# Performance work log

Hardware: AMD Instinct MI355X
Metric: run time of the kernel (lower is better)

Reference implementation:

```python
import jax, jax.numpy as jnp
import numpy as np

B, N, IN_DIM = 2, 2048, 512
D_MODEL, N_HEADS, N_CLASSES = 1024, 16, 1024


def sin_pos_encoding(n, d):
    # Matches SinPositionalEncoding buffer pe[:n]
    pos = jnp.arange(n, dtype=jnp.float32)[:, None]
    div = jnp.exp(jnp.arange(0, d, 2, dtype=jnp.float32) * (-np.log(10000.0) / d))
    pe = jnp.zeros((n, d), dtype=jnp.float32)
    pe = pe.at[:, 0::2].set(jnp.sin(pos * div))
    pe = pe.at[:, 1::2].set(jnp.cos(pos * div))
    return pe


def setup_inputs() -> dict:
    key = jax.random.key(0)
    ks = jax.random.split(key, 9)
    s_emb = (2.0 / (IN_DIM + D_MODEL)) ** 0.5
    s_qk = (2.0 / (2 * D_MODEL)) ** 0.5
    s_v = (2.0 / (D_MODEL + 1)) ** 0.5
    s_o = (2.0 / (N_HEADS + D_MODEL)) ** 0.5
    s_dec = (2.0 / (D_MODEL + N_CLASSES)) ** 0.5
    return {
        'X': jax.random.normal(ks[0], (B, N, IN_DIM), dtype=jnp.float32),
        'emb_w': jax.random.normal(ks[1], (IN_DIM, D_MODEL), dtype=jnp.float32) * s_emb,
        'emb_b': jax.random.normal(ks[2], (D_MODEL,), dtype=jnp.float32) * 0.01,
        'Wq': jax.random.normal(ks[3], (N_HEADS, D_MODEL, D_MODEL), dtype=jnp.float32) * s_qk,
        'Wk': jax.random.normal(ks[4], (N_HEADS, D_MODEL, D_MODEL), dtype=jnp.float32) * s_qk,
        'Wv': jax.random.normal(ks[5], (N_HEADS, D_MODEL, 1), dtype=jnp.float32) * s_v,
        'Wo': jax.random.normal(ks[6], (N_HEADS, D_MODEL), dtype=jnp.float32) * s_o,
        'dec_w': jax.random.normal(ks[7], (D_MODEL, N_CLASSES), dtype=jnp.float32) * s_dec,
        'dec_b': jax.random.normal(ks[8], (N_CLASSES,), dtype=jnp.float32) * 0.01,
    }


def reference(X, emb_w, emb_b, Wq, Wk, Wv, Wo, dec_w, dec_b):
    b, n, _ = X.shape
    d = emb_w.shape[1]
    h = X @ emb_w + emb_b                       # [b, n, d]
    h = h + sin_pos_encoding(n, d)[None]        # positional encoding
    Q = jnp.einsum('bnd,hde->bhne', h, Wq)      # [b, H, n, d]
    K = jnp.einsum('bnd,hde->bhne', h, Wk)      # [b, H, n, d]
    V = jnp.einsum('bnd,hdv->bhnv', h, Wv)      # [b, H, n, 1]
    scores = jnp.einsum('bhqe,bhke->bhqk', Q, K) / jnp.sqrt(jnp.float32(d))
    # mask[:, 0] = 1 is applied MULTIPLICATIVELY before softmax: column 0 -> 0
    scores = scores.at[..., 0].set(0.0)
    attn = jax.nn.softmax(scores, axis=-1)      # [b, H, n, n]
    ctx = jnp.einsum('bhqk,bhkv->bhqv', attn, V)  # [b, H, n, 1]
    ctx = jnp.transpose(ctx, (0, 2, 1, 3)).reshape(b, n, -1)  # [b, n, H]
    out = ctx @ Wo                              # [b, n, d]
    out = out @ dec_w + dec_b                   # [b, n, n_classes]
    return out
```

## Files before the change

kernel.cpp:

```cpp
#include <hip/hip_runtime.h>
#include <cstdint>

typedef __attribute__((ext_vector_type(8))) short bf16x8;
typedef __attribute__((ext_vector_type(4))) float f32x4;

#define B_ 2
#define N_ 2048
#define IN_DIM_ 512
#define D_ 1024
#define H_ 16

__device__ __forceinline__ unsigned short f2bf(float f) {
  uint32_t u = __float_as_uint(f);
  u = u + 0x7fffu + ((u >> 16) & 1u);
  return (unsigned short)(u >> 16);
}
__device__ __forceinline__ float bf2f(unsigned short b) {
  return __uint_as_float(((uint32_t)b) << 16);
}

__device__ __forceinline__ void gll16(const void* g, void* l) {
  __builtin_amdgcn_global_load_lds(
      (const __attribute__((address_space(1))) uint32_t*)g,
      (__attribute__((address_space(3))) uint32_t*)l, 16, 0, 0);
}

__global__ __launch_bounds__(256) void prep_kernel(
    const float* __restrict__ X, unsigned short* __restrict__ Xbf,
    const float* __restrict__ emb_w, unsigned short* __restrict__ EbT) {
  __shared__ float t[32][33];
  const int tid = threadIdx.x;
  if (blockIdx.x < 2048) {
    const int i = (blockIdx.x * 256 + tid) * 4;
    if (i + 3 < B_ * N_ * IN_DIM_) {
      f32x4 v = *(const f32x4*)(X + i);
      uint32_t p0 = (uint32_t)f2bf(v[0]) | ((uint32_t)f2bf(v[1]) << 16);
      uint32_t p1 = (uint32_t)f2bf(v[2]) | ((uint32_t)f2bf(v[3]) << 16);
      *(uint32_t*)(Xbf + i) = p0;
      *(uint32_t*)(Xbf + i + 2) = p1;
    }
  } else {
    const int tb = blockIdx.x - 2048;
    const int bx = tb & 31, by = tb >> 5;
    const int tx = tid & 31, ty = tid >> 5;
    const int x = bx * 32 + tx;
    const int y = by * 32 + ty;
    #pragma unroll
    for (int i = 0; i < 4; ++i)
      t[ty + i * 8][tx] = emb_w[(size_t)(y + i * 8) * D_ + x];
    __syncthreads();
    const int ox = by * 32 + tx;
    #pragma unroll
    for (int i = 0; i < 4; ++i) {
      const int oy = bx * 32 + ty + i * 8;
      EbT[(size_t)oy * IN_DIM_ + ox] = f2bf(t[tx][ty + i * 8]);
    }
  }
}

__global__ __launch_bounds__(256) void cast_bf16x2(const float* __restrict__ X0,
                                                   const float* __restrict__ X1,
                                                   unsigned short* __restrict__ O0,
                                                   unsigned short* __restrict__ O1, int n) {
  int i = (blockIdx.x * 256 + threadIdx.x) * 4;
  const bool second = (i >= n);
  const int j = second ? i - n : i;
  const float* X = second ? X1 : X0;
  unsigned short* O = second ? O1 : O0;
  f32x4 v = *(const f32x4*)(X + j);
  uint32_t p0 = (uint32_t)f2bf(v[0]) | ((uint32_t)f2bf(v[1]) << 16);
  uint32_t p1 = (uint32_t)f2bf(v[2]) | ((uint32_t)f2bf(v[3]) << 16);
  *(uint32_t*)(O + j) = p0;
  *(uint32_t*)(O + j + 2) = p1;
}

__global__ __launch_bounds__(256) void gemm_embed(
    const unsigned short* __restrict__ Xbf, const unsigned short* __restrict__ EbT,
    const float* __restrict__ emb_b, unsigned short* __restrict__ Hbf) {
  const int tid = threadIdx.x, l = tid & 63, w = tid >> 6;
  const int wm = w >> 1, wn = w & 1;
  const int bm = blockIdx.y * 128, bn = blockIdx.x * 128;
  __shared__ unsigned short As[128 * 32], Bs[128 * 32];
  const unsigned short* Ab = Xbf + (size_t)bm * IN_DIM_;
  const unsigned short* Bb = EbT + (size_t)bn * IN_DIM_;
  f32x4 acc[4][4] = {};
  const int lr = l >> 2, lc = (l & 3) * 8;
  for (int k0 = 0; k0 < IN_DIM_; k0 += 32) {
    #pragma unroll
    for (int i = 0; i < 2; ++i) {
      const int c = w * 2 + i;
      gll16(Ab + (size_t)(c * 16 + lr) * IN_DIM_ + k0 + lc, As + c * 512);
      gll16(Bb + (size_t)(c * 16 + lr) * IN_DIM_ + k0 + lc, Bs + c * 512);
    }
    __syncthreads();
    bf16x8 af[4], bfr[4];
    #pragma unroll
    for (int f = 0; f < 4; ++f) {
      af[f]  = *(const bf16x8*)(As + (wm * 64 + f * 16 + (l & 15)) * 32 + (l >> 4) * 8);
      bfr[f] = *(const bf16x8*)(Bs + (wn * 64 + f * 16 + (l & 15)) * 32 + (l >> 4) * 8);
    }
    #pragma unroll
    for (int fr = 0; fr < 4; ++fr)
      #pragma unroll
      for (int fc = 0; fc < 4; ++fc)
        acc[fr][fc] = __builtin_amdgcn_mfma_f32_16x16x32_bf16(af[fr], bfr[fc], acc[fr][fc], 0, 0, 0);
    __syncthreads();
  }
  const float kF = -0.017988946039015983f;
  #pragma unroll
  for (int fr = 0; fr < 4; ++fr) {
    #pragma unroll
    for (int fc = 0; fc < 4; ++fc) {
      const int col = bn + wn * 64 + fc * 16 + (l & 15);
      const float eb = emb_b[col];
      const float fac = expf((float)(col >> 1) * kF);
      #pragma unroll
      for (int j = 0; j < 4; ++j) {
        const int row = bm + wm * 64 + fr * 16 + (l >> 4) * 4 + j;
        const float pos = (float)(row & (N_ - 1));
        const float ang = pos * fac;
        const float pe = (col & 1) ? cosf(ang) : sinf(ang);
        float v = acc[fr][fc][j] + eb + pe;
        float o = __shfl_xor(v, 1);
        unsigned short mb = f2bf(v), ob = f2bf(o);
        uint32_t pk = (l & 1) ? ((uint32_t)ob | ((uint32_t)mb << 16))
                              : ((uint32_t)mb | ((uint32_t)ob << 16));
        const bool mine = (l & 1) ? (j >= 2) : (j < 2);
        if (mine)
          *(uint32_t*)(Hbf + (size_t)row * D_ + (col & ~1)) = pk;
      }
    }
  }
}

__global__ __launch_bounds__(512, 2) void gemm_nt256(
    const unsigned short* __restrict__ A, const unsigned short* __restrict__ Bm,
    unsigned short* __restrict__ O, int K, long aZ, long bZ, long oZ,
    int nbx, int nby, int ldo) {
  extern __shared__ unsigned short KQ[];
  const int nb = gridDim.x;
  const int bid = blockIdx.x;
  const int wid = (bid & 7) * (nb >> 3) + (bid >> 3);
  const int bxi = wid % nbx;
  const int rest = wid / nbx;
  const int byi = rest % nby;
  const int z = rest / nby;
  const int tid = threadIdx.x;
  const int l = tid & 63, l15 = l & 15, l7 = l & 7, lq = l >> 4;
  const int wv = tid >> 6, wm = wv >> 2, wn = wv & 3;
  const unsigned short* Ab = A + (size_t)z * aZ + (size_t)(byi * 256) * K;
  const unsigned short* Bb = Bm + (size_t)z * bZ + (size_t)(bxi * 256) * K;

  const int srow = tid >> 3, spc = tid & 7, scol = (spc ^ (srow & 7)) * 8;
  auto stageU = [&](const unsigned short* src, int rowBase, int k0, unsigned short* ldsU) {
    gll16(src + (size_t)(rowBase + srow) * K + k0 + scol, ldsU + tid * 8);
  };

  {
    unsigned short* A0 = KQ;
    unsigned short* B0 = KQ + 16384;
    stageU(Bb, 0, 0, B0); stageU(Bb, 64, 0, B0 + 4096);
    stageU(Bb, 128, 0, B0 + 8192); stageU(Bb, 192, 0, B0 + 12288);
    stageU(Ab, 0, 0, A0); stageU(Ab, 128, 0, A0 + 8192);
    stageU(Ab, 64, 0, A0 + 4096); stageU(Ab, 192, 0, A0 + 12288);
  }
  __builtin_amdgcn_sched_barrier(0);
  asm volatile("s_waitcnt vmcnt(2)" ::: "memory");
  __builtin_amdgcn_s_barrier();
  __builtin_amdgcn_sched_barrier(0);

  f32x4 acc[8][4] = {};
  const int arow0 = wm * 128 + l15;
  const int brow0 = wn * 64 + l15;
  const int nt = K >> 6;

  for (int t = 0; t < nt; ++t) {
    unsigned short* Acur = KQ + (t & 1) * 32768;
    unsigned short* Bcur = Acur + 16384;
    unsigned short* Anxt = KQ + ((t & 1) ^ 1) * 32768;
    unsigned short* Bnxt = Anxt + 16384;
    const int k0n = (t + 1) * 64;
    const bool more = (t < nt - 1);
    bf16x8 bfr[4][2];
    #pragma unroll
    for (int r = 0; r < 4; ++r) {
      if (r == 0) {
        #pragma unroll
        for (int fc = 0; fc < 4; ++fc)
          #pragma unroll
          for (int kh = 0; kh < 2; ++kh)
            bfr[fc][kh] = *(const bf16x8*)(Bcur + (brow0 + fc * 16) * 64 +
                                           (((kh * 4 + lq) ^ l7) * 8));
      }
      bf16x8 af[2][2];
      #pragma unroll
      for (int i = 0; i < 2; ++i)
        #pragma unroll
        for (int kh = 0; kh < 2; ++kh)
          af[i][kh] = *(const bf16x8*)(Acur + (arow0 + (2 * r + i) * 16) * 64 +
                                       (((kh * 4 + lq) ^ l7) * 8));
      if (more) {
        if (r == 0)      { stageU(Bb, 0, k0n, Bnxt);          stageU(Bb, 64, k0n, Bnxt + 4096); }
        else if (r == 1) { stageU(Bb, 128, k0n, Bnxt + 8192); stageU(Bb, 192, k0n, Bnxt + 12288); }
        else if (r == 2) { stageU(Ab, 0, k0n, Anxt);          stageU(Ab, 128, k0n, Anxt + 8192); }
        else             { stageU(Ab, 64, k0n, Anxt + 4096);  stageU(Ab, 192, k0n, Anxt + 12288); }
      }
      __builtin_amdgcn_sched_barrier(0);
      if (r == 1) {
        if (t == nt - 1) asm volatile("s_waitcnt vmcnt(0)" ::: "memory");
        else             asm volatile("s_waitcnt vmcnt(4)" ::: "memory");
      }
      if (r == 3 && more) asm volatile("s_waitcnt vmcnt(2)" ::: "memory");
      __builtin_amdgcn_s_barrier();
      __builtin_amdgcn_sched_barrier(0);
      __builtin_amdgcn_s_setprio(1);
      #pragma unroll
      for (int i = 0; i < 2; ++i)
        #pragma unroll
        for (int fc = 0; fc < 4; ++fc)
          #pragma unroll
          for (int kh = 0; kh < 2; ++kh)
            acc[2 * r + i][fc] = __builtin_amdgcn_mfma_f32_16x16x32_bf16(
                af[i][kh], bfr[fc][kh], acc[2 * r + i][fc], 0, 0, 0);
      __builtin_amdgcn_s_setprio(0);
      __builtin_amdgcn_sched_barrier(0);
      __builtin_amdgcn_s_barrier();
      __builtin_amdgcn_sched_barrier(0);
    }
  }

  unsigned short* obase = O + (size_t)z * oZ + (size_t)(byi * 256) * ldo + bxi * 256;
  #pragma unroll
  for (int fr = 0; fr < 8; ++fr) {
    #pragma unroll
    for (int fc = 0; fc < 4; ++fc) {
      const int col = wn * 64 + fc * 16 + l15;
      #pragma unroll
      for (int j = 0; j < 4; ++j) {
        const int row = wm * 128 + fr * 16 + lq * 4 + j;
        float v = acc[fr][fc][j];
        float o = __shfl_xor(v, 1);
        unsigned short mb = f2bf(v), ob = f2bf(o);
        uint32_t pk = (l & 1) ? ((uint32_t)ob | ((uint32_t)mb << 16))
                              : ((uint32_t)mb | ((uint32_t)ob << 16));
        const bool mine = (l & 1) ? (j >= 2) : (j < 2);
        if (mine)
          *(uint32_t*)(obase + (size_t)row * ldo + (col & ~1)) = pk;
      }
    }
  }
}

__global__ __launch_bounds__(256) void v_wodec_kernel(
    const unsigned short* __restrict__ Hbf, const float* __restrict__ Wv,
    float* __restrict__ V, const float* __restrict__ Wo,
    const float* __restrict__ dec_w, float* __restrict__ M) {
  if (blockIdx.x < 1024) {
    const int l = threadIdx.x & 63, w = threadIdx.x >> 6;
    const int ng = blockIdx.x * 4 + w;
    const int b = ng >> 11, n = ng & (N_ - 1);
    const unsigned short* hr = Hbf + (size_t)ng * D_;
    float hv[16];
    #pragma unroll
    for (int i = 0; i < 2; ++i) {
      bf16x8 x = *(const bf16x8*)(hr + l * 16 + i * 8);
      #pragma unroll
      for (int j = 0; j < 8; ++j) hv[i * 8 + j] = bf2f((unsigned short)x[j]);
    }
    for (int h = 0; h < H_; ++h) {
      const float* wr = Wv + (size_t)h * D_ + l * 16;
      float s = 0.f;
      #pragma unroll
      for (int i = 0; i < 4; ++i) {
        f32x4 w4 = *(const f32x4*)(wr + i * 4);
        s += hv[i*4+0]*w4[0] + hv[i*4+1]*w4[1] + hv[i*4+2]*w4[2] + hv[i*4+3]*w4[3];
      }
      #pragma unroll
      for (int m = 1; m < 64; m <<= 1) s += __shfl_xor(s, m);
      if (l == 0) V[((size_t)b * H_ + h) * N_ + n] = s;
    }
  } else {
    const int idx = (blockIdx.x - 1024) * 256 + threadIdx.x;
    const int h = idx >> 10, c = idx & 1023;
    float s = 0.f;
    #pragma unroll 4
    for (int d = 0; d < D_; ++d) s += Wo[h * D_ + d] * dec_w[(size_t)d * 1024 + c];
    M[idx] = s;
  }
}

__global__ __launch_bounds__(512, 2) void score_flash(
    const unsigned short* __restrict__ G, const unsigned short* __restrict__ Hb,
    const float* __restrict__ V, float* __restrict__ Pp) {
  extern __shared__ unsigned short KQ[];
  const int bid = blockIdx.x;
  const int wid = (bid & 7) * 128 + (bid >> 3);
  const int kt = wid & 7, qt = (wid >> 3) & 7, h = wid >> 6;
  const int tid = threadIdx.x;
  const int l = tid & 63, l15 = l & 15, l7 = l & 7, lq = l >> 4;
  const int wv = tid >> 6, wm = wv >> 2, wn = wv & 3;
  const unsigned short* Ab = G + ((size_t)h * N_ + qt * 256) * D_;
  const unsigned short* Bb = Hb + (size_t)(kt * 256) * D_;
  const float* Vf = V + (size_t)h * N_;

  const int srow = tid >> 3, spc = tid & 7, scol = (spc ^ (srow & 7)) * 8;
  auto stageU = [&](const unsigned short* src, int rowBase, int k0, unsigned short* ldsU) {
    gll16(src + (size_t)(rowBase + srow) * D_ + k0 + scol, ldsU + tid * 8);
  };

  float vv[4];
  #pragma unroll
  for (int fc = 0; fc < 4; ++fc)
    vv[fc] = Vf[kt * 256 + wn * 64 + fc * 16 + l15];

  {
    unsigned short* A0 = KQ;
    unsigned short* B0 = KQ + 16384;
    stageU(Bb, 0, 0, B0); stageU(Bb, 64, 0, B0 + 4096);
    stageU(Bb, 128, 0, B0 + 8192); stageU(Bb, 192, 0, B0 + 12288);
    stageU(Ab, 0, 0, A0); stageU(Ab, 128, 0, A0 + 8192);
    stageU(Ab, 64, 0, A0 + 4096); stageU(Ab, 192, 0, A0 + 12288);
  }
  __builtin_amdgcn_sched_barrier(0);
  asm volatile("s_waitcnt vmcnt(2)" ::: "memory");
  __builtin_amdgcn_s_barrier();
  __builtin_amdgcn_sched_barrier(0);

  f32x4 acc[8][4] = {};
  const int arow0 = wm * 128 + l15;
  const int brow0 = wn * 64 + l15;

  for (int t = 0; t < 16; ++t) {
    unsigned short* Acur = KQ + (t & 1) * 32768;
    unsigned short* Bcur = Acur + 16384;
    unsigned short* Anxt = KQ + ((t & 1) ^ 1) * 32768;
    unsigned short* Bnxt = Anxt + 16384;
    const int k0n = (t + 1) * 64;
    const bool more = (t < 15);
    bf16x8 bfr[4][2];
    #pragma unroll
    for (int r = 0; r < 4; ++r) {
      if (r == 0) {
        #pragma unroll
        for (int fc = 0; fc < 4; ++fc)
          #pragma unroll
          for (int kh = 0; kh < 2; ++kh)
            bfr[fc][kh] = *(const bf16x8*)(Bcur + (brow0 + fc * 16) * 64 +
                                           (((kh * 4 + lq) ^ l7) * 8));
      }
      bf16x8 af[2][2];
      #pragma unroll
      for (int i = 0; i < 2; ++i)
        #pragma unroll
        for (int kh = 0; kh < 2; ++kh)
          af[i][kh] = *(const bf16x8*)(Acur + (arow0 + (2 * r + i) * 16) * 64 +
                                       (((kh * 4 + lq) ^ l7) * 8));
      if (more) {
        if (r == 0)      { stageU(Bb, 0, k0n, Bnxt);          stageU(Bb, 64, k0n, Bnxt + 4096); }
        else if (r == 1) { stageU(Bb, 128, k0n, Bnxt + 8192); stageU(Bb, 192, k0n, Bnxt + 12288); }
        else if (r == 2) { stageU(Ab, 0, k0n, Anxt);          stageU(Ab, 128, k0n, Anxt + 8192); }
        else             { stageU(Ab, 64, k0n, Anxt + 4096);  stageU(Ab, 192, k0n, Anxt + 12288); }
      }
      __builtin_amdgcn_sched_barrier(0);
      if (r == 1) {
        if (t == 15) asm volatile("s_waitcnt vmcnt(0)" ::: "memory");
        else         asm volatile("s_waitcnt vmcnt(4)" ::: "memory");
      }
      if (r == 3 && more) asm volatile("s_waitcnt vmcnt(2)" ::: "memory");
      __builtin_amdgcn_s_barrier();
      __builtin_amdgcn_sched_barrier(0);
      __builtin_amdgcn_s_setprio(1);
      #pragma unroll
      for (int i = 0; i < 2; ++i)
        #pragma unroll
        for (int fc = 0; fc < 4; ++fc)
          #pragma unroll
          for (int kh = 0; kh < 2; ++kh)
            acc[2 * r + i][fc] = __builtin_amdgcn_mfma_f32_16x16x32_bf16(
                af[i][kh], bfr[fc][kh], acc[2 * r + i][fc], 0, 0, 0);
      __builtin_amdgcn_s_setprio(0);
      __builtin_amdgcn_sched_barrier(0);
      __builtin_amdgcn_s_barrier();
      __builtin_amdgcn_sched_barrier(0);
    }
  }

  __syncthreads();
  float* sb = (float*)KQ;
  #pragma unroll
  for (int fr = 0; fr < 8; ++fr) {
    #pragma unroll
    for (int j = 0; j < 4; ++j) {
      float s4[4];
      #pragma unroll
      for (int fc = 0; fc < 4; ++fc) s4[fc] = acc[fr][fc][j] * 0.03125f;
      if (kt == 0 && wn == 0 && l15 == 0) s4[0] = 0.0f;
      float ps = 0.f, pv = 0.f;
      #pragma unroll
      for (int fc = 0; fc < 4; ++fc) {
        const float e = __expf(s4[fc] - 8.0f);
        ps += e; pv += e * vv[fc];
      }
      ps += __shfl_xor(ps, 1); pv += __shfl_xor(pv, 1);
      ps += __shfl_xor(ps, 2); pv += __shfl_xor(pv, 2);
      ps += __shfl_xor(ps, 4); pv += __shfl_xor(pv, 4);
      ps += __shfl_xor(ps, 8); pv += __shfl_xor(pv, 8);
      if (l15 == 0) {
        const int q = wm * 128 + fr * 16 + lq * 4 + j;
        sb[(q * 4 + wn) * 2 + 0] = ps;
        sb[(q * 4 + wn) * 2 + 1] = pv;
      }
    }
  }
  __syncthreads();
  if (tid < 256) {
    const int q = tid;
    float L = 0.f, O = 0.f;
    #pragma unroll
    for (int n = 0; n < 4; ++n) { L += sb[(q * 4 + n) * 2]; O += sb[(q * 4 + n) * 2 + 1]; }
    float* p = Pp + (((size_t)h * 8 + kt) * N_ + qt * 256 + q) * 2;
    p[0] = L; p[1] = O;
  }
}

__global__ __launch_bounds__(256) void merge8(const float* __restrict__ Pp,
                                              float* __restrict__ ctx) {
  const int idx = blockIdx.x * 256 + threadIdx.x;
  const int h = idx >> 11, q = idx & (N_ - 1);
  float L = 0.f, O = 0.f;
  #pragma unroll
  for (int kt = 0; kt < 8; ++kt) {
    const float* p = Pp + (((size_t)h * 8 + kt) * N_ + q) * 2;
    L += p[0]; O += p[1];
  }
  ctx[(size_t)q * H_ + h] = O / L;
}

__global__ __launch_bounds__(256) void final_kernel(
    const float* __restrict__ ctx, const float* __restrict__ M,
    const float* __restrict__ dec_b, float* __restrict__ out) {
  const int idx = blockIdx.x * 256 + threadIdx.x;
  const int c = idx & 1023;
  const float* cr = ctx + (size_t)(idx >> 10) * H_;
  float s = dec_b[c];
  #pragma unroll
  for (int h = 0; h < H_; ++h) s += cr[h] * M[h * 1024 + c];
  out[idx] = s;
}

extern "C" void kernel_launch(void* const* d_in, const int* in_sizes, int n_in,
                              void* d_out, int out_size, void* d_ws, size_t ws_size,
                              hipStream_t stream) {
  const float* X     = (const float*)d_in[0];
  const float* emb_w = (const float*)d_in[1];
  const float* emb_b = (const float*)d_in[2];
  const float* Wq    = (const float*)d_in[3];
  const float* Wk    = (const float*)d_in[4];
  const float* Wv    = (const float*)d_in[5];
  const float* Wo    = (const float*)d_in[6];
  const float* dec_b = (const float*)d_in[8];
  const float* dec_w = (const float*)d_in[7];
  float* out = (float*)d_out;
  (void)in_sizes; (void)n_in; (void)out_size;

  char* ws = (char*)d_ws;
  unsigned short* Hbf = (unsigned short*)(ws);
  unsigned short* Wkq = (unsigned short*)(ws + ((size_t)8 << 20));
  float* Vb  = (float*)(ws + ((size_t)40 << 20));
  float* ctx = (float*)(ws + ((size_t)40 << 20) + ((size_t)256 << 10));
  float* Mw  = (float*)(ws + ((size_t)40 << 20) + ((size_t)512 << 10));
  char* S = ws + ((size_t)41 << 20);
  unsigned short* Xbf  = (unsigned short*)(S);
  unsigned short* EbT  = (unsigned short*)(S + ((size_t)4 << 20));
  unsigned short* Wqbf = (unsigned short*)(S);
  unsigned short* Wkbf = (unsigned short*)(S + ((size_t)32 << 20));
  unsigned short* G    = (unsigned short*)(S);
  float* Pp = (float*)d_out;

  const size_t need = ((size_t)41 << 20) + ((size_t)64 << 20);
  if (ws_size < need) return;

  prep_kernel<<<2560, 256, 0, stream>>>(X, Xbf, emb_w, EbT);
  gemm_embed<<<dim3(8, 32), 256, 0, stream>>>(Xbf, EbT, emb_b, Hbf);
  cast_bf16x2<<<32768, 256, 0, stream>>>(Wq, Wk, Wqbf, Wkbf, H_ * D_ * D_);
  gemm_nt256<<<256, 512, 131072, stream>>>(Wkbf, Wqbf, Wkq, D_,
                                           (long)D_ * D_, (long)D_ * D_, (long)D_ * D_,
                                           4, 4, 1024);
  v_wodec_kernel<<<1088, 256, 0, stream>>>(Hbf, Wv, Vb, Wo, dec_w, Mw);

  for (int b = 0; b < B_; ++b) {
    const unsigned short* Hb = Hbf + (size_t)b * N_ * D_;
    gemm_nt256<<<512, 512, 131072, stream>>>(Hb, Wkq, G, D_,
                                             0L, (long)D_ * D_, (long)N_ * D_,
                                             4, 8, 1024);
    score_flash<<<1024, 512, 131072, stream>>>(G, Hb, Vb + (size_t)b * H_ * N_, Pp);
    merge8<<<128, 256, 0, stream>>>(Pp, ctx + (size_t)b * N_ * H_);
  }
  final_kernel<<<16384, 256, 0, stream>>>(ctx, Mw, dec_b, out);
}
```

Baseline: 699.6 us.

## Process two key tiles per score_flash block with mid-loop epilogue

Each score_flash block now walks two consecutive 256-key tiles in one 32-step pipelined loop, halving the grid from 1024 to 512 blocks. After step 15 it runs the softmax/V reduction epilogue for the first tile, using a separate LDS scratch region so the already-issued prefetch of the second tile's data is not clobbered. It then resets the accumulators and continues. The aim is to amortize block prologue/pipeline fill and hide epilogue work behind in-flight loads, at the cost of extra LDS (139264 bytes) and a longer serial block.

```diff
diff --git a/kernel.cpp b/kernel.cpp
--- a/kernel.cpp
+++ b/kernel.cpp
@@ -294,13 +294,14 @@
     const float* __restrict__ V, float* __restrict__ Pp) {
   extern __shared__ unsigned short KQ[];
   const int bid = blockIdx.x;
-  const int wid = (bid & 7) * 128 + (bid >> 3);
-  const int kt = wid & 7, qt = (wid >> 3) & 7, h = wid >> 6;
+  const int wid = (bid & 7) * 64 + (bid >> 3);
+  const int ktp = wid & 3, qt = (wid >> 2) & 7, h = wid >> 5;
   const int tid = threadIdx.x;
   const int l = tid & 63, l15 = l & 15, l7 = l & 7, lq = l >> 4;
   const int wv = tid >> 6, wm = wv >> 2, wn = wv & 3;
   const unsigned short* Ab = G + ((size_t)h * N_ + qt * 256) * D_;
-  const unsigned short* Bb = Hb + (size_t)(kt * 256) * D_;
+  const unsigned short* Bb0 = Hb + (size_t)(ktp * 512) * D_;
+  const unsigned short* Bb1 = Bb0 + (size_t)256 * D_;
   const float* Vf = V + (size_t)h * N_;
 
   const int srow = tid >> 3, spc = tid & 7, scol = (spc ^ (srow & 7)) * 8;
@@ -308,16 +309,63 @@
     gll16(src + (size_t)(rowBase + srow) * D_ + k0 + scol, ldsU + tid * 8);
   };
 
-  float vv[4];
+  float vvA[4], vvB[4];
   #pragma unroll
-  for (int fc = 0; fc < 4; ++fc)
-    vv[fc] = Vf[kt * 256 + wn * 64 + fc * 16 + l15];
+  for (int fc = 0; fc < 4; ++fc) {
+    vvA[fc] = Vf[ktp * 512 + wn * 64 + fc * 16 + l15];
+    vvB[fc] = Vf[ktp * 512 + 256 + wn * 64 + fc * 16 + l15];
+  }
+
+  f32x4 acc[8][4] = {};
+  const int arow0 = wm * 128 + l15;
+  const int brow0 = wn * 64 + l15;
+
+  auto epi = [&](int p) {
+    const int ktg = ktp * 2 + p;
+    float* sb = (float*)(KQ + 65536);
+    #pragma unroll
+    for (int fr = 0; fr < 8; ++fr) {
+      #pragma unroll
+      for (int j = 0; j < 4; ++j) {
+        float s4[4];
+        #pragma unroll
+        for (int fc = 0; fc < 4; ++fc) s4[fc] = acc[fr][fc][j] * 0.03125f;
+        if (ktg == 0 && wn == 0 && l15 == 0) s4[0] = 0.0f;
+        float ps = 0.f, pv = 0.f;
+        #pragma unroll
+        for (int fc = 0; fc < 4; ++fc) {
+          const float e = __expf(s4[fc] - 8.0f);
+          ps += e; pv += e * (p ? vvB[fc] : vvA[fc]);
+        }
+        ps += __shfl_xor(ps, 1); pv += __shfl_xor(pv, 1);
+        ps += __shfl_xor(ps, 2); pv += __shfl_xor(pv, 2);
+        ps += __shfl_xor(ps, 4); pv += __shfl_xor(pv, 4);
+        ps += __shfl_xor(ps, 8); pv += __shfl_xor(pv, 8);
+        if (l15 == 0) {
+          const int q = wm * 128 + fr * 16 + lq * 4 + j;
+          sb[(q * 4 + wn) * 2 + 0] = ps;
+          sb[(q * 4 + wn) * 2 + 1] = pv;
+        }
+      }
+    }
+    asm volatile("s_waitcnt lgkmcnt(0)" ::: "memory");
+    __builtin_amdgcn_s_barrier();
+    __builtin_amdgcn_sched_barrier(0);
+    if (tid < 256) {
+      const int q = tid;
+      float L = 0.f, O = 0.f;
+      #pragma unroll
+      for (int n = 0; n < 4; ++n) { L += sb[(q * 4 + n) * 2]; O += sb[(q * 4 + n) * 2 + 1]; }
+      float* pp = Pp + (((size_t)h * 8 + ktg) * N_ + qt * 256 + q) * 2;
+      pp[0] = L; pp[1] = O;
+    }
+  };
 
   {
     unsigned short* A0 = KQ;
     unsigned short* B0 = KQ + 16384;
-    stageU(Bb, 0, 0, B0); stageU(Bb, 64, 0, B0 + 4096);
-    stageU(Bb, 128, 0, B0 + 8192); stageU(Bb, 192, 0, B0 + 12288);
+    stageU(Bb0, 0, 0, B0); stageU(Bb0, 64, 0, B0 + 4096);
+    stageU(Bb0, 128, 0, B0 + 8192); stageU(Bb0, 192, 0, B0 + 12288);
     stageU(Ab, 0, 0, A0); stageU(Ab, 128, 0, A0 + 8192);
     stageU(Ab, 64, 0, A0 + 4096); stageU(Ab, 192, 0, A0 + 12288);
   }
@@ -326,17 +374,14 @@
   __builtin_amdgcn_s_barrier();
   __builtin_amdgcn_sched_barrier(0);
 
-  f32x4 acc[8][4] = {};
-  const int arow0 = wm * 128 + l15;
-  const int brow0 = wn * 64 + l15;
-
-  for (int t = 0; t < 16; ++t) {
+  for (int t = 0; t < 32; ++t) {
     unsigned short* Acur = KQ + (t & 1) * 32768;
     unsigned short* Bcur = Acur + 16384;
     unsigned short* Anxt = KQ + ((t & 1) ^ 1) * 32768;
     unsigned short* Bnxt = Anxt + 16384;
-    const int k0n = (t + 1) * 64;
-    const bool more = (t < 15);
+    const int k0n = ((t + 1) & 15) * 64;
+    const unsigned short* Bst = (t >= 15) ? Bb1 : Bb0;
+    const bool more = (t < 31);
     bf16x8 bfr[4][2];
     #pragma unroll
     for (int r = 0; r < 4; ++r) {
@@ -356,14 +401,14 @@
           af[i][kh] = *(const bf16x8*)(Acur + (arow0 + (2 * r + i) * 16) * 64 +
                                        (((kh * 4 + lq) ^ l7) * 8));
       if (more) {
-        if (r == 0)      { stageU(Bb, 0, k0n, Bnxt);          stageU(Bb, 64, k0n, Bnxt + 4096); }
-        else if (r == 1) { stageU(Bb, 128, k0n, Bnxt + 8192); stageU(Bb, 192, k0n, Bnxt + 12288); }
-        else if (r == 2) { stageU(Ab, 0, k0n, Anxt);          stageU(Ab, 128, k0n, Anxt + 8192); }
-        else             { stageU(Ab, 64, k0n, Anxt + 4096);  stageU(Ab, 192, k0n, Anxt + 12288); }
+        if (r == 0)      { stageU(Bst, 0, k0n, Bnxt);          stageU(Bst, 64, k0n, Bnxt + 4096); }
+        else if (r == 1) { stageU(Bst, 128, k0n, Bnxt + 8192); stageU(Bst, 192, k0n, Bnxt + 12288); }
+        else if (r == 2) { stageU(Ab, 0, k0n, Anxt);           stageU(Ab, 128, k0n, Anxt + 8192); }
+        else             { stageU(Ab, 64, k0n, Anxt + 4096);   stageU(Ab, 192, k0n, Anxt + 12288); }
       }
       __builtin_amdgcn_sched_barrier(0);
       if (r == 1) {
-        if (t == 15) asm volatile("s_waitcnt vmcnt(0)" ::: "memory");
+        if (t == 31) asm volatile("s_waitcnt vmcnt(0)" ::: "memory");
         else         asm volatile("s_waitcnt vmcnt(4)" ::: "memory");
       }
       if (r == 3 && more) asm volatile("s_waitcnt vmcnt(2)" ::: "memory");
@@ -383,44 +428,16 @@
       __builtin_amdgcn_s_barrier();
       __builtin_amdgcn_sched_barrier(0);
     }
-  }
-
-  __syncthreads();
-  float* sb = (float*)KQ;
-  #pragma unroll
-  for (int fr = 0; fr < 8; ++fr) {
-    #pragma unroll
-    for (int j = 0; j < 4; ++j) {
-      float s4[4];
-      #pragma unroll
-      for (int fc = 0; fc < 4; ++fc) s4[fc] = acc[fr][fc][j] * 0.03125f;
-      if (kt == 0 && wn == 0 && l15 == 0) s4[0] = 0.0f;
-      float ps = 0.f, pv = 0.f;
-      #pragma unroll
-      for (int fc = 0; fc < 4; ++fc) {
-        const float e = __expf(s4[fc] - 8.0f);
-        ps += e; pv += e * vv[fc];
-      }
-      ps += __shfl_xor(ps, 1); pv += __shfl_xor(pv, 1);
-      ps += __shfl_xor(ps, 2); pv += __shfl_xor(pv, 2);
-      ps += __shfl_xor(ps, 4); pv += __shfl_xor(pv, 4);
-      ps += __shfl_xor(ps, 8); pv += __shfl_xor(pv, 8);
-      if (l15 == 0) {
-        const int q = wm * 128 + fr * 16 + lq * 4 + j;
-        sb[(q * 4 + wn) * 2 + 0] = ps;
-        sb[(q * 4 + wn) * 2 + 1] = pv;
-      }
-    }
-  }
-  __syncthreads();
-  if (tid < 256) {
-    const int q = tid;
-    float L = 0.f, O = 0.f;
-    #pragma unroll
-    for (int n = 0; n < 4; ++n) { L += sb[(q * 4 + n) * 2]; O += sb[(q * 4 + n) * 2 + 1]; }
-    float* p = Pp + (((size_t)h * 8 + kt) * N_ + qt * 256 + q) * 2;
-    p[0] = L; p[1] = O;
-  }
+    if (t == 15) {
+      epi(0);
+      #pragma unroll
+      for (int fr = 0; fr < 8; ++fr)
+        #pragma unroll
+        for (int fc = 0; fc < 4; ++fc)
+          acc[fr][fc] = f32x4{0.f, 0.f, 0.f, 0.f};
+    }
+  }
+  epi(1);
 }
 
 __global__ __launch_bounds__(256) void merge8(const float* __restrict__ Pp,
@@ -493,7 +510,7 @@
     gemm_nt256<<<512, 512, 131072, stream>>>(Hb, Wkq, G, D_,
                                              0L, (long)D_ * D_, (long)N_ * D_,
                                              4, 8, 1024);
-    score_flash<<<1024, 512, 131072, stream>>>(G, Hb, Vb + (size_t)b * H_ * N_, Pp);
+    score_flash<<<512, 512, 139264, stream>>>(G, Hb, Vb + (size_t)b * H_ * N_, Pp);
     merge8<<<128, 256, 0, stream>>>(Pp, ctx + (size_t)b * N_ * H_);
   }
   final_kernel<<<16384, 256, 0, stream>>>(ctx, Mw, dec_b, out);
```

Measured after the change: 719.5 us. 1.03x slower.
